# Performance work log

Hardware: AMD Instinct MI355X
Metric: run time of the kernel (lower is better)

## Reference

```python
import jax, jax.numpy as jnp
import numpy as np

B, L, D = 8192, 2048, 256


def setup_inputs() -> dict:
    key = jax.random.key(0)
    kx, kl = jax.random.split(key)
    x = jax.random.normal(kx, (B, D), dtype=jnp.float32)
    landmarks = jax.random.normal(kl, (L, D), dtype=jnp.float32)
    return {"x": x, "landmarks": landmarks}


def reference(x, landmarks):
    # RBF layer: out[b, l] = exp(-gamma * sum_d (landmarks[l, d] - x[b, d])^2)
    # gamma='auto' -> 1 / n_features (landmarks.shape[1])
    gamma = jnp.float32(1.0 / landmarks.shape[1])
    # avoids materializing the [B, L, D] broadcast-diff intermediate)
    x2 = jnp.sum(x * x, axis=-1, keepdims=True)          # [B, 1]
    l2 = jnp.sum(landmarks * landmarks, axis=-1)         # [L]
    cross = jnp.einsum('bd,ld->bl', x, landmarks)        # [B, L]
    d2 = jnp.maximum(x2 + l2[None, :] - 2.0 * cross, 0.0)
    return jnp.exp(-gamma * d2)
```

## Files before the change

### kernel.cpp

```cpp
#include <hip/hip_runtime.h>


typedef __bf16 bf16x8 __attribute__((ext_vector_type(8)));
typedef float  f32x4  __attribute__((ext_vector_type(4)));

#define B_ROWS 8192
#define L_ROWS 2048
#define K_DIM  256

#define GLD_LDS(g, l) __builtin_amdgcn_global_load_lds(                      \
    (const __attribute__((address_space(1))) void*)(g),                      \
    (__attribute__((address_space(3))) void*)(l), 16, 0, 0)

__device__ __forceinline__ unsigned short f32_to_bf16_rne(float f) {
    union { float f; unsigned int u; } v; v.f = f;
    unsigned int u = v.u;
    unsigned int r = (u + 0x7fffu + ((u >> 16) & 1u)) >> 16;
    return (unsigned short)r;
}

__global__ __launch_bounds__(256) void cvt_rows_kernel(
    const float* __restrict__ in, unsigned short* __restrict__ outb,
    float* __restrict__ sq)
{
    const int lane = threadIdx.x & 63;
    const int row  = blockIdx.x * 4 + (threadIdx.x >> 6);
    const float4 v = ((const float4*)(in + row * K_DIM))[lane];
    ushort4 o;
    o.x = f32_to_bf16_rne(v.x);
    o.y = f32_to_bf16_rne(v.y);
    o.z = f32_to_bf16_rne(v.z);
    o.w = f32_to_bf16_rne(v.w);
    ((ushort4*)(outb + row * K_DIM))[lane] = o;
    float s = v.x*v.x + v.y*v.y + v.z*v.z + v.w*v.w;
    #pragma unroll
    for (int off = 32; off > 0; off >>= 1) s += __shfl_down(s, off, 64);
    if (lane == 0) sq[row] = s;
}

__global__ __launch_bounds__(256) void rbf_gemm_kernel(
    const unsigned short* __restrict__ A,
    const unsigned short* __restrict__ Bm,
    const float* __restrict__ x2,
    const float* __restrict__ l2,
    float* __restrict__ out)
{
    __shared__ unsigned short As[128 * 64];
    __shared__ unsigned short Bs[128 * 64];

    const int tid  = threadIdx.x;
    const int wave = tid >> 6;
    const int lane = tid & 63;
    const int wm = wave >> 1, wn = wave & 1;
    const int bm = blockIdx.x, bn = blockIdx.y;

    f32x4 acc[4][4];
    #pragma unroll
    for (int i = 0; i < 4; ++i)
        #pragma unroll
        for (int j = 0; j < 4; ++j)
            acc[i][j] = (f32x4){0.f, 0.f, 0.f, 0.f};

    const int ldrow = lane >> 3;
    const int ldcol = (lane & 7) * 8;

    const unsigned short* Ab = A  + (bm * 128) * K_DIM;
    const unsigned short* Bb = Bm + (bn * 128) * K_DIM;

    for (int k0 = 0; k0 < K_DIM; k0 += 64) {
        #pragma unroll
        for (int it = 0; it < 4; ++it) {
            const int r = wave * 32 + it * 8;
            GLD_LDS(Ab + (r + ldrow) * K_DIM + k0 + ldcol, &As[r * 64]);
            GLD_LDS(Bb + (r + ldrow) * K_DIM + k0 + ldcol, &Bs[r * 64]);
        }
        __syncthreads();

        #pragma unroll
        for (int kk = 0; kk < 64; kk += 32) {
            const int ko = kk + (lane >> 4) * 8;
            bf16x8 af[4], bfr[4];
            #pragma unroll
            for (int t = 0; t < 4; ++t) {
                af[t]  = *(const bf16x8*)&As[(wm*64 + t*16 + (lane & 15)) * 64 + ko];
                bfr[t] = *(const bf16x8*)&Bs[(wn*64 + t*16 + (lane & 15)) * 64 + ko];
            }
            #pragma unroll
            for (int mt = 0; mt < 4; ++mt)
                #pragma unroll
                for (int nt = 0; nt < 4; ++nt)
                    acc[mt][nt] = __builtin_amdgcn_mfma_f32_16x16x32_bf16(
                        af[mt], bfr[nt], acc[mt][nt], 0, 0, 0);
        }
        __syncthreads();
    }

    const float gamma = 1.0f / 256.0f;
    const int col0 = bn * 128 + wn * 64 + (lane & 15);
    const int row0 = bm * 128 + wm * 64 + (lane >> 4) * 4;
    #pragma unroll
    for (int mt = 0; mt < 4; ++mt) {
        const int rb = row0 + mt * 16;
        float xv[4];
        #pragma unroll
        for (int r = 0; r < 4; ++r) xv[r] = x2[rb + r];
        #pragma unroll
        for (int nt = 0; nt < 4; ++nt) {
            const int c  = col0 + nt * 16;
            const float lv = l2[c];
            #pragma unroll
            for (int r = 0; r < 4; ++r) {
                float d2 = fmaxf(xv[r] + lv - 2.0f * acc[mt][nt][r], 0.0f);
                out[(rb + r) * L_ROWS + c] = __expf(-gamma * d2);
            }
        }
    }
}

extern "C" void kernel_launch(void* const* d_in, const int* in_sizes, int n_in,
                              void* d_out, int out_size, void* d_ws, size_t ws_size,
                              hipStream_t stream) {
    const float* x  = (const float*)d_in[0];
    const float* lm = (const float*)d_in[1];
    float* out = (float*)d_out;

    char* ws = (char*)d_ws;
    unsigned short* xb = (unsigned short*)ws;
    unsigned short* lb = (unsigned short*)(ws + (size_t)B_ROWS*K_DIM*2);
    float* x2 = (float*)(ws + (size_t)B_ROWS*K_DIM*2 + (size_t)L_ROWS*K_DIM*2);
    float* l2 = x2 + B_ROWS;

    cvt_rows_kernel<<<B_ROWS/4, 256, 0, stream>>>(x, xb, x2);
    cvt_rows_kernel<<<L_ROWS/4, 256, 0, stream>>>(lm, lb, l2);
    rbf_gemm_kernel<<<dim3(B_ROWS/128, L_ROWS/128), 256, 0, stream>>>(xb, lb, x2, l2, out);
}
```

Measured before the change: 96.28 us.

## Double-buffer LDS tiles in RBF GEMM and merge conversion kernels

```diff
diff --git a/kernel.cpp b/kernel.cpp
--- a/kernel.cpp
+++ b/kernel.cpp
@@ -20,18 +20,22 @@
 }
 
 __global__ __launch_bounds__(256) void cvt_rows_kernel(
-    const float* __restrict__ in, unsigned short* __restrict__ outb,
-    float* __restrict__ sq)
+    const float* __restrict__ x, const float* __restrict__ lm,
+    unsigned short* __restrict__ xb, unsigned short* __restrict__ lb,
+    float* __restrict__ x2, float* __restrict__ l2)
 {
     const int lane = threadIdx.x & 63;
-    const int row  = blockIdx.x * 4 + (threadIdx.x >> 6);
-    const float4 v = ((const float4*)(in + row * K_DIM))[lane];
+    const int gw   = blockIdx.x * 4 + (threadIdx.x >> 6);
+    const float* in; unsigned short* outb; float* sq; int row;
+    if (gw < B_ROWS) { in = x;  outb = xb; sq = x2; row = gw; }
+    else             { in = lm; outb = lb; sq = l2; row = gw - B_ROWS; }
+    const float4 v = ((const float4*)(in + (size_t)row * K_DIM))[lane];
     ushort4 o;
     o.x = f32_to_bf16_rne(v.x);
     o.y = f32_to_bf16_rne(v.y);
     o.z = f32_to_bf16_rne(v.z);
     o.w = f32_to_bf16_rne(v.w);
-    ((ushort4*)(outb + row * K_DIM))[lane] = o;
+    ((ushort4*)(outb + (size_t)row * K_DIM))[lane] = o;
     float s = v.x*v.x + v.y*v.y + v.z*v.z + v.w*v.w;
     #pragma unroll
     for (int off = 32; off > 0; off >>= 1) s += __shfl_down(s, off, 64);
@@ -45,8 +49,8 @@
     const float* __restrict__ l2,
     float* __restrict__ out)
 {
-    __shared__ unsigned short As[128 * 64];
-    __shared__ unsigned short Bs[128 * 64];
+    __shared__ unsigned short As[2][128 * 64];
+    __shared__ unsigned short Bs[2][128 * 64];
 
     const int tid  = threadIdx.x;
     const int wave = tid >> 6;
@@ -64,26 +68,35 @@
     const int ldrow = lane >> 3;
     const int ldcol = (lane & 7) * 8;
 
-    const unsigned short* Ab = A  + (bm * 128) * K_DIM;
-    const unsigned short* Bb = Bm + (bn * 128) * K_DIM;
+    const unsigned short* Ab = A  + (size_t)(bm * 128) * K_DIM;
+    const unsigned short* Bb = Bm + (size_t)(bn * 128) * K_DIM;
 
-    for (int k0 = 0; k0 < K_DIM; k0 += 64) {
-        #pragma unroll
-        for (int it = 0; it < 4; ++it) {
-            const int r = wave * 32 + it * 8;
-            GLD_LDS(Ab + (r + ldrow) * K_DIM + k0 + ldcol, &As[r * 64]);
-            GLD_LDS(Bb + (r + ldrow) * K_DIM + k0 + ldcol, &Bs[r * 64]);
-        }
-        __syncthreads();
+#define STAGE(buf, k0)                                                       \
+    _Pragma("unroll")                                                        \
+    for (int it = 0; it < 4; ++it) {                                         \
+        const int r = wave * 32 + it * 8;                                    \
+        GLD_LDS(Ab + (r + ldrow) * K_DIM + (k0) + ldcol, &As[buf][r * 64]);  \
+        GLD_LDS(Bb + (r + ldrow) * K_DIM + (k0) + ldcol, &Bs[buf][r * 64]);  \
+    }
+
+    STAGE(0, 0);
+
+    #pragma unroll
+    for (int t = 0; t < 4; ++t) {
+        const int cur = t & 1;
+        if (t < 3) { STAGE(cur ^ 1, (t + 1) * 64); }
+        if (t < 3) asm volatile("s_waitcnt vmcnt(8)" ::: "memory");
+        else       asm volatile("s_waitcnt vmcnt(0)" ::: "memory");
+        asm volatile("s_barrier" ::: "memory");
 
         #pragma unroll
         for (int kk = 0; kk < 64; kk += 32) {
             const int ko = kk + (lane >> 4) * 8;
             bf16x8 af[4], bfr[4];
             #pragma unroll
-            for (int t = 0; t < 4; ++t) {
-                af[t]  = *(const bf16x8*)&As[(wm*64 + t*16 + (lane & 15)) * 64 + ko];
-                bfr[t] = *(const bf16x8*)&Bs[(wn*64 + t*16 + (lane & 15)) * 64 + ko];
+            for (int tt = 0; tt < 4; ++tt) {
+                af[tt]  = *(const bf16x8*)&As[cur][(wm*64 + tt*16 + (lane & 15)) * 64 + ko];
+                bfr[tt] = *(const bf16x8*)&Bs[cur][(wn*64 + tt*16 + (lane & 15)) * 64 + ko];
             }
             #pragma unroll
             for (int mt = 0; mt < 4; ++mt)
@@ -92,8 +105,9 @@
                     acc[mt][nt] = __builtin_amdgcn_mfma_f32_16x16x32_bf16(
                         af[mt], bfr[nt], acc[mt][nt], 0, 0, 0);
         }
-        __syncthreads();
+        if (t < 3) asm volatile("s_barrier" ::: "memory");
     }
+#undef STAGE
 
     const float gamma = 1.0f / 256.0f;
     const int col0 = bn * 128 + wn * 64 + (lane & 15);
@@ -111,7 +125,7 @@
             #pragma unroll
             for (int r = 0; r < 4; ++r) {
                 float d2 = fmaxf(xv[r] + lv - 2.0f * acc[mt][nt][r], 0.0f);
-                out[(rb + r) * L_ROWS + c] = __expf(-gamma * d2);
+                out[(size_t)(rb + r) * L_ROWS + c] = __expf(-gamma * d2);
             }
         }
     }
@@ -130,7 +144,6 @@
     float* x2 = (float*)(ws + (size_t)B_ROWS*K_DIM*2 + (size_t)L_ROWS*K_DIM*2);
     float* l2 = x2 + B_ROWS;
 
-    cvt_rows_kernel<<<B_ROWS/4, 256, 0, stream>>>(x, xb, x2);
-    cvt_rows_kernel<<<L_ROWS/4, 256, 0, stream>>>(lm, lb, l2);
+    cvt_rows_kernel<<<(B_ROWS + L_ROWS)/4, 256, 0, stream>>>(x, lm, xb, lb, x2, l2);
     rbf_gemm_kernel<<<dim3(B_ROWS/128, L_ROWS/128), 256, 0, stream>>>(xb, lb, x2, l2, out);
 }
```

Measured after the change: 91.79 us. 1.05x faster.
